# Kernel optimization log

Hardware: AMD Instinct MI355X
Metric: run time of the kernel (lower is better)

The kernel has to match this reference:

```python
import jax, jax.numpy as jnp
import numpy as np

T, NP, NA, NV = 8, 16000, 16000, 200
DIN, H, KA, L = 256, 256, 4, 5
YEARS_TRAIN = (5, 6, 7)
BETA, EPS = 0.5, 1.0
SQRT2 = 1.4142135623730951


def setup_inputs() -> dict:
    key = jax.random.key(0)
    ks = jax.random.split(key, 24)
    s = 0.05
    return {
        'x_paper': jax.random.normal(ks[0], (T, NP, DIN), jnp.float32),
        'x_author': jax.random.normal(ks[1], (T, NA, DIN), jnp.float32),
        'x_venue': jax.random.normal(ks[2], (T, NV, DIN), jnp.float32),
        'neigh_author_idx': jax.random.randint(ks[3], (NP, KA), 0, NA),
        'neigh_venue_idx': jax.random.randint(ks[4], (NP,), 0, NV),
        'y_true': jax.random.uniform(ks[5], (len(YEARS_TRAIN), NP, L), jnp.float32, 0.0, 50.0),
        'W_paper': s * jax.random.normal(ks[6], (DIN, H), jnp.float32),
        'b_paper': jnp.zeros((H,), jnp.float32),
        'W_author': s * jax.random.normal(ks[7], (DIN, H), jnp.float32),
        'b_author': jnp.zeros((H,), jnp.float32),
        'W_venue': s * jax.random.normal(ks[8], (DIN, H), jnp.float32),
        'b_venue': jnp.zeros((H,), jnp.float32),
        'w_meta': jax.random.normal(ks[9], (3,), jnp.float32),
        'Wx': s * jax.random.normal(ks[10], (H, 3 * H), jnp.float32),
        'Wh': s * jax.random.normal(ks[11], (H, 3 * H), jnp.float32),
        'b_gru': jnp.zeros((3 * H,), jnp.float32),
        'W_eta': s * jax.random.normal(ks[12], (H, 1), jnp.float32),
        'b_eta': jnp.zeros((1,), jnp.float32),
        'W_mu': s * jax.random.normal(ks[13], (H, 1), jnp.float32),
        'b_mu': jnp.zeros((1,), jnp.float32),
        'W_sigma': s * jax.random.normal(ks[14], (H, 1), jnp.float32),
        'b_sigma': jnp.zeros((1,), jnp.float32),
    }


def reference(x_paper, x_author, x_venue, neigh_author_idx, neigh_venue_idx, y_true,
              W_paper, b_paper, W_author, b_author, W_venue, b_venue, w_meta,
              Wx, Wh, b_gru, W_eta, b_eta, W_mu, b_mu, W_sigma, b_sigma):
    # --- encoder: per-type linear + ReLU over all T snapshots ---
    emb_p = jax.nn.relu(jnp.einsum('tnd,dh->tnh', x_paper, W_paper) + b_paper)   # [T,NP,H]
    emb_a = jax.nn.relu(jnp.einsum('tnd,dh->tnh', x_author, W_author) + b_author)  # [T,NA,H]
    emb_v = jax.nn.relu(jnp.einsum('tnd,dh->tnh', x_venue, W_venue) + b_venue)   # [T,NV,H]

    # --- temporal smoothing regulariser L_time (all nodes common across years) ---
    l_time = jnp.mean(jnp.stack([
        jnp.mean(jnp.sum((e[1:] - e[:-1]) ** 2, axis=-1)) for e in (emb_p, emb_a, emb_v)
    ]))

    # --- weighted imputer, batched over all papers and all years ---
    w = jax.nn.softmax(w_meta)
    auth_mean = jnp.mean(emb_a[:, neigh_author_idx], axis=2)   # [T,NP,H]
    ven = emb_v[:, neigh_venue_idx]                            # [T,NP,H]
    v_all = w[0] * auth_mean + w[1] * ven + w[2] * emb_p       # [T,NP,H]

    # --- build lookback sequences V_p for all train years at once ---
    yrs = np.array([[t - k for k in range(1, L + 1)] for t in YEARS_TRAIN])  # [3,L]
    V = jnp.transpose(v_all[yrs], (0, 2, 1, 3)).reshape(-1, L, H)  # [B=3*NP, L, H]
    B = V.shape[0]

    # --- ImpactRNN: GRU over the lookback sequence ---
    def gru_step(h, x):
        gx = x @ Wx + b_gru
        gh = h @ Wh
        xr, xz, xn = jnp.split(gx, 3, axis=-1)
        hr, hz, hn = jnp.split(gh, 3, axis=-1)
        r = jax.nn.sigmoid(xr + hr)
        z = jax.nn.sigmoid(xz + hz)
        n = jnp.tanh(xn + r * hn)
        return (1.0 - z) * n + z * h, None

    h0 = jnp.zeros((B, H), V.dtype)
    h_last, _ = jax.lax.scan(gru_step, h0, jnp.swapaxes(V, 0, 1))

    eta = jax.nn.softplus(h_last @ W_eta + b_eta)              # [B,1]
    mu = h_last @ W_mu + b_mu                                  # [B,1]
    sigma = jax.nn.softplus(h_last @ W_sigma + b_sigma) + 1e-3  # [B,1]

    # --- cumulative log-normal citation curve, then per-horizon increments ---
    horizons = jnp.arange(1.0, L + 1.0, dtype=V.dtype)
    zscore = (jnp.log(horizons)[None, :] - mu) / (sigma * SQRT2)
    y_cum = eta * 0.5 * (1.0 + jax.lax.erf(zscore))            # [B,L]
    y_hat = jnp.concatenate([y_cum[:, :1], y_cum[:, 1:] - y_cum[:, :-1]], axis=1)

    l_pred = jnp.mean((jnp.log1p(y_true.reshape(-1, L) + EPS) - jnp.log1p(y_hat)) ** 2)
    return l_pred + BETA * l_time
```

## Files before the change

kernel.cpp:

```cpp
#include <hip/hip_runtime.h>
#include <cmath>

#define NP  16000
#define NV  200
#define HH  256

typedef short short8 __attribute__((ext_vector_type(8)));
typedef float f32x4  __attribute__((ext_vector_type(4)));

__device__ __forceinline__ unsigned short f2b(float f) {
  union { float f; unsigned u; } x; x.f = f;
  unsigned r = x.u + 0x7fffu + ((x.u >> 16) & 1u);
  return (unsigned short)(r >> 16);
}
__device__ __forceinline__ float b2f(unsigned short h) {
  union { unsigned u; float f; } x; x.u = ((unsigned)h) << 16;
  return x.f;
}
__device__ __forceinline__ float b2f_lo(unsigned u) {
  union { unsigned v; float f; } x; x.v = u << 16; return x.f;
}
__device__ __forceinline__ float b2f_hi(unsigned u) {
  union { unsigned v; float f; } x; x.v = u & 0xffff0000u; return x.f;
}
__device__ __forceinline__ unsigned cvt2(float a, float b) {
  unsigned r;
  asm("v_cvt_pk_bf16_f32 %0, %1, %2" : "=v"(r) : "v"(a), "v"(b));
  return r;
}
__device__ __forceinline__ void gld16(const void* g, void* l) {
  __builtin_amdgcn_global_load_lds((const __attribute__((address_space(1))) void*)g,
                                   (__attribute__((address_space(3))) void*)l, 16, 0, 0);
}
__device__ __forceinline__ float sigm(float x) { return 1.f / (1.f + __expf(-x)); }
__device__ __forceinline__ float tanhfast(float x) {
  const float e = __expf(-2.f * fabsf(x));
  const float t = (1.f - e) / (1.f + e);
  return x < 0.f ? -t : t;
}
__device__ __forceinline__ int xcd_swz(int orig, int q, int r) {
  const int xcd = orig & 7, loc = orig >> 3;
  return (xcd < r ? xcd * (q + 1) : r * (q + 1) + (xcd - r) * q) + loc;
}

__global__ __launch_bounds__(256) void packWt(const float* __restrict__ W,
                                              unsigned short* __restrict__ Wt) {
  const int n = blockIdx.x, k = threadIdx.x;
  Wt[n * 256 + k] = f2b(W[k * 256 + n]);
}
__global__ __launch_bounds__(256) void packW2t(const float* __restrict__ Wx,
                                               const float* __restrict__ Wh,
                                               unsigned short* __restrict__ W2t) {
  const int col = blockIdx.x;
  for (int k = threadIdx.x; k < 512; k += 256)
    W2t[(size_t)col * 512 + k] =
        f2b(k < 256 ? Wx[(size_t)k * 768 + col] : Wh[(size_t)(k - 256) * 768 + col]);
}

__global__ __launch_bounds__(512, 2) void embed_all(
    const float* __restrict__ Xp, const float* __restrict__ Xa, const float* __restrict__ Xv,
    const unsigned short* __restrict__ Wtp, const unsigned short* __restrict__ Wta,
    const unsigned short* __restrict__ Wtv,
    const float* __restrict__ bp, const float* __restrict__ ba, const float* __restrict__ bvn,
    unsigned short* __restrict__ Ep, unsigned short* __restrict__ Ea,
    unsigned short* __restrict__ Ev) {
  __shared__ __align__(16) unsigned short lds[24576];
  unsigned short* As = lds;
  unsigned short* Bs = lds + 8192;
  const int t = threadIdx.x, w = t >> 6, l = t & 63;
  const int bid = blockIdx.x;
  const float* Xf; const unsigned short* Wt; const float* bias; unsigned short* E;
  int M, m0;
  if (bid < 1000)      { Xf = Xp; Wt = Wtp; bias = bp;  E = Ep; M = 128000; m0 = bid * 128; }
  else if (bid < 2000) { Xf = Xa; Wt = Wta; bias = ba;  E = Ea; M = 128000; m0 = (bid - 1000) * 128; }
  else                 { Xf = Xv; Wt = Wtv; bias = bvn; E = Ev; M = 1600;   m0 = (bid - 2000) * 128; }
  const int srow = l >> 3, scol = ((l & 7) ^ srow) * 8;
  const int wr = w >> 2, wc = w & 3;
  const int arow = t >> 2, acg = t & 3;
  const int agrow = min(m0 + arow, M - 1);
  const float* aptr = Xf + (size_t)agrow * 256 + acg * 16;

  f32x4 acc[4][4];
#pragma unroll
  for (int i = 0; i < 4; ++i)
#pragma unroll
    for (int j = 0; j < 4; ++j) acc[i][j] = {0.f, 0.f, 0.f, 0.f};

  float4 areg0, areg1, areg2, areg3;
  areg0 = *reinterpret_cast<const float4*>(aptr + 0);
  areg1 = *reinterpret_cast<const float4*>(aptr + 4);
  areg2 = *reinterpret_cast<const float4*>(aptr + 8);
  areg3 = *reinterpret_cast<const float4*>(aptr + 12);

#pragma unroll
  for (int c = 0; c < 4; ++c) {
#pragma unroll
    for (int i = 0; i < 4; ++i) {
      const int seg = 4 * w + i;
      gld16(Wt + (size_t)(8 * seg + srow) * 256 + c * 64 + scol, (void*)(Bs + seg * 512));
    }
    {
      uint4 u0, u1;
      u0.x = cvt2(areg0.x, areg0.y); u0.y = cvt2(areg0.z, areg0.w);
      u0.z = cvt2(areg1.x, areg1.y); u0.w = cvt2(areg1.z, areg1.w);
      u1.x = cvt2(areg2.x, areg2.y); u1.y = cvt2(areg2.z, areg2.w);
      u1.z = cvt2(areg3.x, areg3.y); u1.w = cvt2(areg3.z, areg3.w);
      const int s0 = (acg * 2) ^ (arow & 7), s1 = (acg * 2 + 1) ^ (arow & 7);
      *reinterpret_cast<uint4*>(As + arow * 64 + s0 * 8) = u0;
      *reinterpret_cast<uint4*>(As + arow * 64 + s1 * 8) = u1;
    }
    if (c < 3) {
      const float* np = aptr + (c + 1) * 64;
      areg0 = *reinterpret_cast<const float4*>(np + 0);
      areg1 = *reinterpret_cast<const float4*>(np + 4);
      areg2 = *reinterpret_cast<const float4*>(np + 8);
      areg3 = *reinterpret_cast<const float4*>(np + 12);
    }
    __syncthreads();
#pragma unroll
    for (int ks = 0; ks < 2; ++ks) {
      short8 av[4], bv[4];
#pragma unroll
      for (int mi = 0; mi < 4; ++mi) {
        const int r = wr * 64 + mi * 16 + (l & 15);
        const int slot = (ks * 4 + (l >> 4)) ^ (r & 7);
        av[mi] = *reinterpret_cast<const short8*>(As + r * 64 + slot * 8);
      }
#pragma unroll
      for (int nj = 0; nj < 4; ++nj) {
        const int r = wc * 64 + nj * 16 + (l & 15);
        const int slot = (ks * 4 + (l >> 4)) ^ (r & 7);
        bv[nj] = *reinterpret_cast<const short8*>(Bs + r * 64 + slot * 8);
      }
#pragma unroll
      for (int mi = 0; mi < 4; ++mi)
#pragma unroll
        for (int nj = 0; nj < 4; ++nj)
          acc[mi][nj] = __builtin_amdgcn_mfma_f32_16x16x32_bf16(av[mi], bv[nj], acc[mi][nj], 0, 0, 0);
    }
    __syncthreads();
  }

  unsigned short* ep = lds + w * 2560;
  const int grow = m0 + wr * 64 + l;
#pragma unroll
  for (int p = 0; p < 2; ++p) {
#pragma unroll
    for (int nj2 = 0; nj2 < 2; ++nj2) {
      const int nj = 2 * p + nj2;
      const int colg = wc * 64 + nj * 16 + (l & 15);
      const float bvv = bias[colg];
#pragma unroll
      for (int mi = 0; mi < 4; ++mi)
#pragma unroll
        for (int e = 0; e < 4; ++e) {
          const int rl = mi * 16 + (l >> 4) * 4 + e;
          ep[rl * 40 + nj2 * 16 + (l & 15)] = f2b(fmaxf(acc[mi][nj][e] + bvv, 0.f));
        }
    }
    __syncthreads();
    if (grow < M) {
#pragma unroll
      for (int j = 0; j < 4; ++j) {
        const uint4 v = *reinterpret_cast<const uint4*>(ep + l * 40 + j * 8);
        *reinterpret_cast<uint4*>(E + (size_t)grow * 256 + wc * 64 + p * 32 + j * 8) = v;
      }
    }
    __syncthreads();
  }
}

__global__ __launch_bounds__(256, 2) void gx_gemm(const unsigned short* __restrict__ Abf,
                                                  const unsigned short* __restrict__ W2t,
                                                  const float* __restrict__ bias,
                                                  unsigned short* __restrict__ GX) {
  __shared__ __align__(16) unsigned short lds[16384];
  unsigned short* As = lds;
  unsigned short* Bs = lds + 8192;
  const int t = threadIdx.x, w = t >> 6, l = t & 63;
  const int work = xcd_swz(blockIdx.x, 656, 2);
  const int m0 = (work / 6) * 128, n0 = (work % 6) * 128;
  const int srow = l >> 3;
  const int scol = ((l & 7) ^ srow) * 8;
  f32x4 acc[4][4];
#pragma unroll
  for (int i = 0; i < 4; ++i)
#pragma unroll
    for (int j = 0; j < 4; ++j) acc[i][j] = {0.f, 0.f, 0.f, 0.f};
  const int mrow0 = 64 * (w >> 1), ncol0 = 64 * (w & 1);

#pragma unroll
  for (int c = 0; c < 4; ++c) {
#pragma unroll
    for (int i = 0; i < 4; ++i) {
      const int seg = 4 * w + i;
      gld16(Abf + (size_t)(m0 + 8 * seg + srow) * 256 + c * 64 + scol, (void*)(As + seg * 512));
    }
#pragma unroll
    for (int i = 0; i < 4; ++i) {
      const int seg = 4 * w + i;
      gld16(W2t + (size_t)(n0 + 8 * seg + srow) * 512 + c * 64 + scol, (void*)(Bs + seg * 512));
    }
    __syncthreads();
#pragma unroll
    for (int ks = 0; ks < 2; ++ks) {
      short8 av[4], bv[4];
#pragma unroll
      for (int mi = 0; mi < 4; ++mi) {
        const int r = mrow0 + mi * 16 + (l & 15);
        const int slot = (ks * 4 + (l >> 4)) ^ (r & 7);
        av[mi] = *reinterpret_cast<const short8*>(As + r * 64 + slot * 8);
      }
#pragma unroll
      for (int nj = 0; nj < 4; ++nj) {
        const int r = ncol0 + nj * 16 + (l & 15);
        const int slot = (ks * 4 + (l >> 4)) ^ (r & 7);
        bv[nj] = *reinterpret_cast<const short8*>(Bs + r * 64 + slot * 8);
      }
#pragma unroll
      for (int mi = 0; mi < 4; ++mi)
#pragma unroll
        for (int nj = 0; nj < 4; ++nj)
          acc[mi][nj] = __builtin_amdgcn_mfma_f32_16x16x32_bf16(av[mi], bv[nj], acc[mi][nj], 0, 0, 0);
    }
    __syncthreads();
  }
  unsigned short* ep = lds + w * 2560;
  const int grow = m0 + mrow0 + l;
#pragma unroll
  for (int p = 0; p < 2; ++p) {
#pragma unroll
    for (int nj2 = 0; nj2 < 2; ++nj2) {
      const int nj = 2 * p + nj2;
      const int colg = n0 + ncol0 + nj * 16 + (l & 15);
      const float bvv = bias[colg];
#pragma unroll
      for (int mi = 0; mi < 4; ++mi)
#pragma unroll
        for (int e = 0; e < 4; ++e) {
          const int rl = mi * 16 + (l >> 4) * 4 + e;
          ep[rl * 40 + nj2 * 16 + (l & 15)] = f2b(acc[mi][nj][e] + bvv);
        }
    }
    __syncthreads();
#pragma unroll
    for (int j = 0; j < 4; ++j) {
      const uint4 v = *reinterpret_cast<const uint4*>(ep + l * 40 + j * 8);
      *reinterpret_cast<uint4*>(GX + (size_t)grow * 768 + n0 + ncol0 + p * 32 + j * 8) = v;
    }
    __syncthreads();
  }
}

__global__ __launch_bounds__(256) void ltime_kernel(const unsigned short* __restrict__ ep,
                                                    const unsigned short* __restrict__ ea,
                                                    const unsigned short* __restrict__ ev,
                                                    float* __restrict__ partials) {
  const unsigned PO = 3584000u, VO = 44800u;
  const unsigned TOT = 2u * PO + VO;
  const unsigned SL = 512000u, SLV = 6400u;
  const float wbig = 1.f / (3.f * 7.f * 16000.f);
  const float wsmall = 1.f / (3.f * 7.f * 200.f);
  float local = 0.f;
  for (unsigned i = blockIdx.x * 256u + threadIdx.x; i < TOT; i += gridDim.x * 256u) {
    const unsigned short* base; unsigned off, sl; float wgt;
    if (i < 2u * PO) { base = (i < PO) ? ep : ea; off = (i < PO) ? i : i - PO; sl = SL; wgt = wbig; }
    else             { base = ev; off = i - 2u * PO; sl = SLV; wgt = wsmall; }
    const uint4 u0 = *reinterpret_cast<const uint4*>(base + (size_t)off * 8);
    const uint4 u1 = *reinterpret_cast<const uint4*>(base + (size_t)(off + sl) * 8);
    float s = 0.f, d;
    d = b2f_lo(u1.x) - b2f_lo(u0.x); s += d * d;
    d = b2f_hi(u1.x) - b2f_hi(u0.x); s += d * d;
    d = b2f_lo(u1.y) - b2f_lo(u0.y); s += d * d;
    d = b2f_hi(u1.y) - b2f_hi(u0.y); s += d * d;
    d = b2f_lo(u1.z) - b2f_lo(u0.z); s += d * d;
    d = b2f_hi(u1.z) - b2f_hi(u0.z); s += d * d;
    d = b2f_lo(u1.w) - b2f_lo(u0.w); s += d * d;
    d = b2f_hi(u1.w) - b2f_hi(u0.w); s += d * d;
    local += wgt * s;
  }
  __shared__ float red[256];
  red[threadIdx.x] = local;
  __syncthreads();
  for (int s = 128; s > 0; s >>= 1) {
    if (threadIdx.x < s) red[threadIdx.x] += red[threadIdx.x + s];
    __syncthreads();
  }
  if (threadIdx.x == 0) partials[blockIdx.x] = red[0];
}

__global__ __launch_bounds__(256) void vall_kernel(const unsigned short* __restrict__ ep,
                                                   const unsigned short* __restrict__ ea,
                                                   const unsigned short* __restrict__ ev,
                                                   const int* __restrict__ aidx,
                                                   const int* __restrict__ vidx,
                                                   const float* __restrict__ wm,
                                                   unsigned short* __restrict__ vall) {
  const int w = threadIdx.x >> 6, l = threadIdx.x & 63;
  const int n = blockIdx.x * 4 + w;
  float w0 = wm[0], w1 = wm[1], w2 = wm[2];
  const float mx = fmaxf(w0, fmaxf(w1, w2));
  const float e0 = expf(w0 - mx), e1 = expf(w1 - mx), e2 = expf(w2 - mx);
  const float inv = 1.f / (e0 + e1 + e2);
  w0 = e0 * inv; w1 = e1 * inv; w2 = e2 * inv;
  const int a0 = aidx[n * 4 + 0], a1 = aidx[n * 4 + 1];
  const int a2 = aidx[n * 4 + 2], a3 = aidx[n * 4 + 3];
  const int vn = vidx[n];
  const int cb = l * 4;
  for (int t = 0; t < 7; ++t) {
    const size_t tb = (size_t)t * NP * HH;
    const uint2 ua0 = *reinterpret_cast<const uint2*>(ea + tb + (size_t)a0 * HH + cb);
    const uint2 ua1 = *reinterpret_cast<const uint2*>(ea + tb + (size_t)a1 * HH + cb);
    const uint2 ua2 = *reinterpret_cast<const uint2*>(ea + tb + (size_t)a2 * HH + cb);
    const uint2 ua3 = *reinterpret_cast<const uint2*>(ea + tb + (size_t)a3 * HH + cb);
    const uint2 uv  = *reinterpret_cast<const uint2*>(ev + (size_t)t * NV * HH + (size_t)vn * HH + cb);
    const uint2 up  = *reinterpret_cast<const uint2*>(ep + tb + (size_t)n * HH + cb);
    float o[4];
    o[0] = w0 * 0.25f * (b2f_lo(ua0.x) + b2f_lo(ua1.x) + b2f_lo(ua2.x) + b2f_lo(ua3.x)) + w1 * b2f_lo(uv.x) + w2 * b2f_lo(up.x);
    o[1] = w0 * 0.25f * (b2f_hi(ua0.x) + b2f_hi(ua1.x) + b2f_hi(ua2.x) + b2f_hi(ua3.x)) + w1 * b2f_hi(uv.x) + w2 * b2f_hi(up.x);
    o[2] = w0 * 0.25f * (b2f_lo(ua0.y) + b2f_lo(ua1.y) + b2f_lo(ua2.y) + b2f_lo(ua3.y)) + w1 * b2f_lo(uv.y) + w2 * b2f_lo(up.y);
    o[3] = w0 * 0.25f * (b2f_hi(ua0.y) + b2f_hi(ua1.y) + b2f_hi(ua2.y) + b2f_hi(ua3.y)) + w1 * b2f_hi(uv.y) + w2 * b2f_hi(up.y);
    uint2 ov; ov.x = cvt2(o[0], o[1]); ov.y = cvt2(o[2], o[3]);
    *reinterpret_cast<uint2*>(vall + tb + (size_t)n * HH + cb) = ov;
  }
}

__global__ __launch_bounds__(256) void gru_h0(const unsigned short* __restrict__ GX,
                                              unsigned short* __restrict__ H0) {
  const int idx = blockIdx.x * 256 + threadIdx.x;
  const int hrow = idx >> 6, jq = idx & 63;
  const int g = (hrow >= 32000) ? 2 : (hrow >= 16000 ? 1 : 0);
  const int n = hrow - g * 16000;
  const size_t gxrow = (size_t)(4 + g) * 16000 + n;
  const unsigned short* gp = GX + gxrow * 768 + jq * 4;
  const uint2 uz = *reinterpret_cast<const uint2*>(gp + 256);
  const uint2 un = *reinterpret_cast<const uint2*>(gp + 512);
  float h[4];
  h[0] = (1.f - sigm(b2f_lo(uz.x))) * tanhfast(b2f_lo(un.x));
  h[1] = (1.f - sigm(b2f_hi(uz.x))) * tanhfast(b2f_hi(un.x));
  h[2] = (1.f - sigm(b2f_lo(uz.y))) * tanhfast(b2f_lo(un.y));
  h[3] = (1.f - sigm(b2f_hi(uz.y))) * tanhfast(b2f_hi(un.y));
  uint2 o; o.x = cvt2(h[0], h[1]); o.y = cvt2(h[2], h[3]);
  *reinterpret_cast<uint2*>(H0 + (size_t)hrow * 256 + jq * 4) = o;
}

__global__ __launch_bounds__(512, 2) void gru_hstep(const unsigned short* __restrict__ GX,
                                                    const unsigned short* __restrict__ W2t,
                                                    const unsigned short* __restrict__ Hsrc,
                                                    unsigned short* __restrict__ Hdst,
                                                    int lstep) {
  __shared__ __align__(16) unsigned short lds[32768];
  unsigned short* As = lds;
  unsigned short* Bs = lds + 8192;
  const int t = threadIdx.x, w = t >> 6, l = t & 63;
  const int work = xcd_swz(blockIdx.x, 93, 6);
  const int bx = work >> 1, jb = work & 1;
  const int m0 = bx * 128, j0 = jb * 128;
  const int g = bx / 125;
  const size_t gxRowBase = (size_t)(4 + g - lstep) * 16000 + (size_t)(m0 - g * 16000);
  const int srow = l >> 3;
  const int scol = ((l & 7) ^ srow) * 8;
  const int wr = w >> 2, wj = w & 3;
  f32x4 acc[3][4][2];
#pragma unroll
  for (int gate = 0; gate < 3; ++gate)
#pragma unroll
    for (int mi = 0; mi < 4; ++mi)
#pragma unroll
      for (int nj = 0; nj < 2; ++nj) acc[gate][mi][nj] = {0.f, 0.f, 0.f, 0.f};

#pragma unroll
  for (int c = 0; c < 4; ++c) {
#pragma unroll
    for (int i = 0; i < 2; ++i) {
      const int seg = w * 2 + i;
      gld16(Hsrc + (size_t)(m0 + 8 * seg + srow) * 256 + c * 64 + scol, (void*)(As + seg * 512));
    }
#pragma unroll
    for (int i = 0; i < 6; ++i) {
      const int seg = w * 6 + i;
      const int tilerow = 8 * seg + srow;
      const int gate = tilerow >> 7, jj = tilerow & 127;
      gld16(W2t + (size_t)(gate * 256 + j0 + jj) * 512 + 256 + c * 64 + scol,
            (void*)(Bs + seg * 512));
    }
    __syncthreads();
#pragma unroll
    for (int ks = 0; ks < 2; ++ks) {
      short8 av[4];
#pragma unroll
      for (int mi = 0; mi < 4; ++mi) {
        const int r = wr * 64 + mi * 16 + (l & 15);
        const int slot = (ks * 4 + (l >> 4)) ^ (r & 7);
        av[mi] = *reinterpret_cast<const short8*>(As + r * 64 + slot * 8);
      }
#pragma unroll
      for (int gate = 0; gate < 3; ++gate) {
        short8 bv0, bv1;
        {
          const int r0 = gate * 128 + wj * 32 + (l & 15);
          const int s0 = (ks * 4 + (l >> 4)) ^ (r0 & 7);
          bv0 = *reinterpret_cast<const short8*>(Bs + r0 * 64 + s0 * 8);
          const int r1 = r0 + 16;
          const int s1 = (ks * 4 + (l >> 4)) ^ (r1 & 7);
          bv1 = *reinterpret_cast<const short8*>(Bs + r1 * 64 + s1 * 8);
        }
#pragma unroll
        for (int mi = 0; mi < 4; ++mi) {
          acc[gate][mi][0] = __builtin_amdgcn_mfma_f32_16x16x32_bf16(av[mi], bv0, acc[gate][mi][0], 0, 0, 0);
          acc[gate][mi][1] = __builtin_amdgcn_mfma_f32_16x16x32_bf16(av[mi], bv1, acc[gate][mi][1], 0, 0, 0);
        }
      }
    }
    __syncthreads();
  }
  unsigned short* ep = lds + w * 2560;
#pragma unroll
  for (int nj = 0; nj < 2; ++nj) {
    const int jcol = j0 + wj * 32 + nj * 16 + (l & 15);
#pragma unroll
    for (int mi = 0; mi < 4; ++mi) {
#pragma unroll
      for (int e = 0; e < 4; ++e) {
        const int rib = wr * 64 + mi * 16 + (l >> 4) * 4 + e;
        const size_t hidx = (size_t)(m0 + rib) * 256 + jcol;
        const size_t gxoff = (gxRowBase + rib) * 768 + jcol;
        const float aR = acc[0][mi][nj][e] + b2f(GX[gxoff]);
        const float aZ = acc[1][mi][nj][e] + b2f(GX[gxoff + 256]);
        const float hn = acc[2][mi][nj][e];
        const float xn = b2f(GX[gxoff + 512]);
        const float rg = sigm(aR);
        const float zg = sigm(aZ);
        const float ng = tanhfast(xn + rg * hn);
        const float ho = b2f(Hsrc[hidx]);
        const int rl = mi * 16 + (l >> 4) * 4 + e;
        ep[rl * 40 + nj * 16 + (l & 15)] = f2b((1.f - zg) * ng + zg * ho);
      }
    }
  }
  __syncthreads();
  {
    const int grow = m0 + wr * 64 + l;
#pragma unroll
    for (int j = 0; j < 4; ++j) {
      const uint4 v = *reinterpret_cast<const uint4*>(ep + l * 40 + j * 8);
      *reinterpret_cast<uint4*>(Hdst + (size_t)grow * 256 + j0 + wj * 32 + j * 8) = v;
    }
  }
}

__device__ inline float softplusf(float x) { return x > 20.f ? x : log1pf(expf(x)); }

__global__ __launch_bounds__(256) void head_kernel(const unsigned short* __restrict__ Hbuf,
                                                   const float* __restrict__ We, const float* __restrict__ be,
                                                   const float* __restrict__ Wm, const float* __restrict__ bmu,
                                                   const float* __restrict__ Ws, const float* __restrict__ bsg,
                                                   const float* __restrict__ yt,
                                                   float* __restrict__ partials) {
  __shared__ float sWe[256], sWm[256], sWs[256];
  const int t = threadIdx.x;
  sWe[t] = We[t]; sWm[t] = Wm[t]; sWs[t] = Ws[t];
  __syncthreads();
  const int row = blockIdx.x * 256 + t;
  float loss = 0.f;
  if (row < 48000) {
    const unsigned short* h = Hbuf + (size_t)row * HH;
    float pe = 0.f, pm = 0.f, ps = 0.f;
#pragma unroll 4
    for (int k0 = 0; k0 < 256; k0 += 8) {
      const uint4 u = *reinterpret_cast<const uint4*>(h + k0);
      const float hv[8] = {b2f_lo(u.x), b2f_hi(u.x), b2f_lo(u.y), b2f_hi(u.y),
                           b2f_lo(u.z), b2f_hi(u.z), b2f_lo(u.w), b2f_hi(u.w)};
#pragma unroll
      for (int q = 0; q < 8; ++q) {
        const int k = k0 + q;
        pe += hv[q] * sWe[k]; pm += hv[q] * sWm[k]; ps += hv[q] * sWs[k];
      }
    }
    const float eta = softplusf(pe + be[0]);
    const float mu  = pm + bmu[0];
    const float sg  = softplusf(ps + bsg[0]) + 0.001f;
    const float inv = 1.f / (sg * 1.41421356237309515f);
    float prev = 0.f;
#pragma unroll
    for (int hz = 1; hz <= 5; ++hz) {
      const float z  = (logf((float)hz) - mu) * inv;
      const float yc = eta * 0.5f * (1.f + erff(z));
      const float yh = yc - prev; prev = yc;
      const float d  = log1pf(yt[(size_t)row * 5 + (hz - 1)] + 1.0f) - log1pf(yh);
      loss += d * d;
    }
  }
  __shared__ float red[256];
  red[t] = loss;
  __syncthreads();
  for (int s = 128; s > 0; s >>= 1) {
    if (t < s) red[t] += red[t + s];
    __syncthreads();
  }
  if (t == 0) partials[blockIdx.x] = red[0];
}

__global__ __launch_bounds__(256) void final_kernel(const float* __restrict__ lt,
                                                    const float* __restrict__ lp,
                                                    float* __restrict__ out) {
  __shared__ float r1[256], r2[256];
  float s1 = 0.f, s2 = 0.f;
  for (int i = threadIdx.x; i < 1024; i += 256) s1 += lt[i];
  for (int i = threadIdx.x; i < 188; i += 256) s2 += lp[i];
  r1[threadIdx.x] = s1; r2[threadIdx.x] = s2;
  __syncthreads();
  for (int s = 128; s > 0; s >>= 1) {
    if (threadIdx.x < s) { r1[threadIdx.x] += r1[threadIdx.x + s]; r2[threadIdx.x] += r2[threadIdx.x + s]; }
    __syncthreads();
  }
  if (threadIdx.x == 0) out[0] = r2[0] / 240000.f + 0.5f * r1[0];
}

extern "C" void kernel_launch(void* const* d_in, const int* in_sizes, int n_in,
                              void* d_out, int out_size, void* d_ws, size_t ws_size,
                              hipStream_t stream) {
  (void)in_sizes; (void)n_in; (void)out_size; (void)ws_size;
  const float* x_paper  = (const float*)d_in[0];
  const float* x_author = (const float*)d_in[1];
  const float* x_venue  = (const float*)d_in[2];
  const int*   aidx     = (const int*)d_in[3];
  const int*   vidx     = (const int*)d_in[4];
  const float* y_true   = (const float*)d_in[5];
  const float* W_paper  = (const float*)d_in[6];
  const float* b_paper  = (const float*)d_in[7];
  const float* W_author = (const float*)d_in[8];
  const float* b_author = (const float*)d_in[9];
  const float* W_venue  = (const float*)d_in[10];
  const float* b_venue  = (const float*)d_in[11];
  const float* w_meta   = (const float*)d_in[12];
  const float* Wx       = (const float*)d_in[13];
  const float* Wh       = (const float*)d_in[14];
  const float* b_gru    = (const float*)d_in[15];
  const float* W_eta    = (const float*)d_in[16];
  const float* b_eta    = (const float*)d_in[17];
  const float* W_mu     = (const float*)d_in[18];
  const float* b_mu     = (const float*)d_in[19];
  const float* W_sigma  = (const float*)d_in[20];
  const float* b_sigma  = (const float*)d_in[21];

  unsigned short* p = (unsigned short*)d_ws;
  unsigned short* va16 = p;  p += (size_t)7 * NP * 256;
  unsigned short* Hb0  = p;  p += (size_t)48000 * 256;
  unsigned short* Hb1  = p;  p += (size_t)48000 * 256;
  unsigned short* W2t  = p;  p += (size_t)768 * 512;
  unsigned short* GX   = p;  p += (size_t)112000 * 768;
  float* ltp = (float*)p;
  float* lpp = ltp + 1024;
  unsigned short* ep16 = GX;
  unsigned short* ea16 = ep16 + (size_t)8 * NP * 256;
  unsigned short* ev16 = ea16 + (size_t)8 * NP * 256;
  unsigned short* Wtp  = ev16 + (size_t)8 * NV * 256;
  unsigned short* Wta  = Wtp + 65536;
  unsigned short* Wtv  = Wta + 65536;

  packWt<<<256, 256, 0, stream>>>(W_paper,  Wtp);
  packWt<<<256, 256, 0, stream>>>(W_author, Wta);
  packWt<<<256, 256, 0, stream>>>(W_venue,  Wtv);
  packW2t<<<768, 256, 0, stream>>>(Wx, Wh, W2t);

  embed_all<<<2013, 512, 0, stream>>>(x_paper, x_author, x_venue, Wtp, Wta, Wtv,
                                      b_paper, b_author, b_venue, ep16, ea16, ev16);

  ltime_kernel<<<1024, 256, 0, stream>>>(ep16, ea16, ev16, ltp);
  vall_kernel<<<NP / 4, 256, 0, stream>>>(ep16, ea16, ev16, aidx, vidx, w_meta, va16);

  gx_gemm<<<5250, 256, 0, stream>>>(va16, W2t, b_gru, GX);

  gru_h0<<<12000, 256, 0, stream>>>(GX, Hb0);
  gru_hstep<<<750, 512, 0, stream>>>(GX, W2t, Hb0, Hb1, 1);
  gru_hstep<<<750, 512, 0, stream>>>(GX, W2t, Hb1, Hb0, 2);
  gru_hstep<<<750, 512, 0, stream>>>(GX, W2t, Hb0, Hb1, 3);
  gru_hstep<<<750, 512, 0, stream>>>(GX, W2t, Hb1, Hb0, 4);

  head_kernel<<<188, 256, 0, stream>>>(Hb0, W_eta, b_eta, W_mu, b_mu, W_sigma, b_sigma,
                                       y_true, lpp);
  final_kernel<<<1, 256, 0, stream>>>(ltp, lpp, (float*)d_out);
}
```

Baseline: 581.9 us.

## Retile embed and GX GEMMs to 64-row tiles with single-pass epilogue

The embedding GEMM moves from 128x256 tiles to 64x256 tiles, doubling the block count and halving per-wave accumulators and LDS. The GX GEMM moves from 128x128 tiles with 256 threads to 64x256 tiles with 512 threads. Both epilogues now stage the whole tile in padded LDS once and write full rows, replacing the two-pass per-wave staging. The aim is more occupancy and less sync in the epilogue, at the cost of reloading the full B weight tile more often relative to A. The M-bound clamp is dropped; the venue blocks divide exactly into 64-row tiles.

```diff
diff --git a/kernel.cpp b/kernel.cpp
--- a/kernel.cpp
+++ b/kernel.cpp
@@ -57,40 +57,36 @@
         f2b(k < 256 ? Wx[(size_t)k * 768 + col] : Wh[(size_t)(k - 256) * 768 + col]);
 }
 
-__global__ __launch_bounds__(512, 2) void embed_all(
+__global__ __launch_bounds__(512) void embed_all(
     const float* __restrict__ Xp, const float* __restrict__ Xa, const float* __restrict__ Xv,
     const unsigned short* __restrict__ Wtp, const unsigned short* __restrict__ Wta,
     const unsigned short* __restrict__ Wtv,
     const float* __restrict__ bp, const float* __restrict__ ba, const float* __restrict__ bvn,
     unsigned short* __restrict__ Ep, unsigned short* __restrict__ Ea,
     unsigned short* __restrict__ Ev) {
-  __shared__ __align__(16) unsigned short lds[24576];
+  __shared__ __align__(16) unsigned short lds[20480];
   unsigned short* As = lds;
-  unsigned short* Bs = lds + 8192;
+  unsigned short* Bs = lds + 4096;
   const int t = threadIdx.x, w = t >> 6, l = t & 63;
   const int bid = blockIdx.x;
   const float* Xf; const unsigned short* Wt; const float* bias; unsigned short* E;
-  int M, m0;
-  if (bid < 1000)      { Xf = Xp; Wt = Wtp; bias = bp;  E = Ep; M = 128000; m0 = bid * 128; }
-  else if (bid < 2000) { Xf = Xa; Wt = Wta; bias = ba;  E = Ea; M = 128000; m0 = (bid - 1000) * 128; }
-  else                 { Xf = Xv; Wt = Wtv; bias = bvn; E = Ev; M = 1600;   m0 = (bid - 2000) * 128; }
+  int m0;
+  if (bid < 2000)      { Xf = Xp; Wt = Wtp; bias = bp;  E = Ep; m0 = bid * 64; }
+  else if (bid < 4000) { Xf = Xa; Wt = Wta; bias = ba;  E = Ea; m0 = (bid - 2000) * 64; }
+  else                 { Xf = Xv; Wt = Wtv; bias = bvn; E = Ev; m0 = (bid - 4000) * 64; }
   const int srow = l >> 3, scol = ((l & 7) ^ srow) * 8;
-  const int wr = w >> 2, wc = w & 3;
-  const int arow = t >> 2, acg = t & 3;
-  const int agrow = min(m0 + arow, M - 1);
-  const float* aptr = Xf + (size_t)agrow * 256 + acg * 16;
-
-  f32x4 acc[4][4];
-#pragma unroll
-  for (int i = 0; i < 4; ++i)
+  const int wrow = (w >> 2) * 32, wcol = (w & 3) * 64;
+  const int arow = t >> 3, aseg = t & 7;
+  const float* aptr = Xf + (size_t)(m0 + arow) * 256 + aseg * 8;
+
+  f32x4 acc[2][4];
+#pragma unroll
+  for (int i = 0; i < 2; ++i)
 #pragma unroll
     for (int j = 0; j < 4; ++j) acc[i][j] = {0.f, 0.f, 0.f, 0.f};
 
-  float4 areg0, areg1, areg2, areg3;
-  areg0 = *reinterpret_cast<const float4*>(aptr + 0);
-  areg1 = *reinterpret_cast<const float4*>(aptr + 4);
-  areg2 = *reinterpret_cast<const float4*>(aptr + 8);
-  areg3 = *reinterpret_cast<const float4*>(aptr + 12);
+  float4 a0 = *reinterpret_cast<const float4*>(aptr);
+  float4 a1 = *reinterpret_cast<const float4*>(aptr + 4);
 
 #pragma unroll
   for (int c = 0; c < 4; ++c) {
@@ -100,40 +96,35 @@
       gld16(Wt + (size_t)(8 * seg + srow) * 256 + c * 64 + scol, (void*)(Bs + seg * 512));
     }
     {
-      uint4 u0, u1;
-      u0.x = cvt2(areg0.x, areg0.y); u0.y = cvt2(areg0.z, areg0.w);
-      u0.z = cvt2(areg1.x, areg1.y); u0.w = cvt2(areg1.z, areg1.w);
-      u1.x = cvt2(areg2.x, areg2.y); u1.y = cvt2(areg2.z, areg2.w);
-      u1.z = cvt2(areg3.x, areg3.y); u1.w = cvt2(areg3.z, areg3.w);
-      const int s0 = (acg * 2) ^ (arow & 7), s1 = (acg * 2 + 1) ^ (arow & 7);
-      *reinterpret_cast<uint4*>(As + arow * 64 + s0 * 8) = u0;
-      *reinterpret_cast<uint4*>(As + arow * 64 + s1 * 8) = u1;
+      uint4 u;
+      u.x = cvt2(a0.x, a0.y); u.y = cvt2(a0.z, a0.w);
+      u.z = cvt2(a1.x, a1.y); u.w = cvt2(a1.z, a1.w);
+      const int slot = aseg ^ (arow & 7);
+      *reinterpret_cast<uint4*>(As + arow * 64 + slot * 8) = u;
     }
     if (c < 3) {
       const float* np = aptr + (c + 1) * 64;
-      areg0 = *reinterpret_cast<const float4*>(np + 0);
-      areg1 = *reinterpret_cast<const float4*>(np + 4);
-      areg2 = *reinterpret_cast<const float4*>(np + 8);
-      areg3 = *reinterpret_cast<const float4*>(np + 12);
+      a0 = *reinterpret_cast<const float4*>(np);
+      a1 = *reinterpret_cast<const float4*>(np + 4);
     }
     __syncthreads();
 #pragma unroll
     for (int ks = 0; ks < 2; ++ks) {
-      short8 av[4], bv[4];
-#pragma unroll
-      for (int mi = 0; mi < 4; ++mi) {
-        const int r = wr * 64 + mi * 16 + (l & 15);
+      short8 av[2], bv[4];
+#pragma unroll
+      for (int mi = 0; mi < 2; ++mi) {
+        const int r = wrow + mi * 16 + (l & 15);
         const int slot = (ks * 4 + (l >> 4)) ^ (r & 7);
         av[mi] = *reinterpret_cast<const short8*>(As + r * 64 + slot * 8);
       }
 #pragma unroll
       for (int nj = 0; nj < 4; ++nj) {
-        const int r = wc * 64 + nj * 16 + (l & 15);
+        const int r = wcol + nj * 16 + (l & 15);
         const int slot = (ks * 4 + (l >> 4)) ^ (r & 7);
         bv[nj] = *reinterpret_cast<const short8*>(Bs + r * 64 + slot * 8);
       }
 #pragma unroll
-      for (int mi = 0; mi < 4; ++mi)
+      for (int mi = 0; mi < 2; ++mi)
 #pragma unroll
         for (int nj = 0; nj < 4; ++nj)
           acc[mi][nj] = __builtin_amdgcn_mfma_f32_16x16x32_bf16(av[mi], bv[nj], acc[mi][nj], 0, 0, 0);
@@ -141,61 +132,53 @@
     __syncthreads();
   }
 
-  unsigned short* ep = lds + w * 2560;
-  const int grow = m0 + wr * 64 + l;
-#pragma unroll
-  for (int p = 0; p < 2; ++p) {
-#pragma unroll
-    for (int nj2 = 0; nj2 < 2; ++nj2) {
-      const int nj = 2 * p + nj2;
-      const int colg = wc * 64 + nj * 16 + (l & 15);
-      const float bvv = bias[colg];
-#pragma unroll
-      for (int mi = 0; mi < 4; ++mi)
-#pragma unroll
-        for (int e = 0; e < 4; ++e) {
-          const int rl = mi * 16 + (l >> 4) * 4 + e;
-          ep[rl * 40 + nj2 * 16 + (l & 15)] = f2b(fmaxf(acc[mi][nj][e] + bvv, 0.f));
-        }
-    }
-    __syncthreads();
-    if (grow < M) {
-#pragma unroll
-      for (int j = 0; j < 4; ++j) {
-        const uint4 v = *reinterpret_cast<const uint4*>(ep + l * 40 + j * 8);
-        *reinterpret_cast<uint4*>(E + (size_t)grow * 256 + wc * 64 + p * 32 + j * 8) = v;
-      }
-    }
-    __syncthreads();
-  }
-}
-
-__global__ __launch_bounds__(256, 2) void gx_gemm(const unsigned short* __restrict__ Abf,
-                                                  const unsigned short* __restrict__ W2t,
-                                                  const float* __restrict__ bias,
-                                                  unsigned short* __restrict__ GX) {
-  __shared__ __align__(16) unsigned short lds[16384];
+#pragma unroll
+  for (int nj = 0; nj < 4; ++nj) {
+    const int col = wcol + nj * 16 + (l & 15);
+    const float bvv = bias[col];
+#pragma unroll
+    for (int mi = 0; mi < 2; ++mi)
+#pragma unroll
+      for (int e = 0; e < 4; ++e) {
+        const int row = wrow + mi * 16 + (l >> 4) * 4 + e;
+        lds[row * 264 + col] = f2b(fmaxf(acc[mi][nj][e] + bvv, 0.f));
+      }
+  }
+  __syncthreads();
+  {
+    const int r2 = t >> 3, s2 = t & 7;
+    const unsigned short* src = lds + r2 * 264 + s2 * 32;
+    const uint4 v0 = *reinterpret_cast<const uint4*>(src);
+    const uint4 v1 = *reinterpret_cast<const uint4*>(src + 8);
+    const uint4 v2 = *reinterpret_cast<const uint4*>(src + 16);
+    const uint4 v3 = *reinterpret_cast<const uint4*>(src + 24);
+    uint4* dst = reinterpret_cast<uint4*>(E + (size_t)(m0 + r2) * 256 + s2 * 32);
+    dst[0] = v0; dst[1] = v1; dst[2] = v2; dst[3] = v3;
+  }
+}
+
+__global__ __launch_bounds__(512) void gx_gemm(const unsigned short* __restrict__ Abf,
+                                               const unsigned short* __restrict__ W2t,
+                                               const float* __restrict__ bias,
+                                               unsigned short* __restrict__ GX) {
+  __shared__ __align__(16) unsigned short lds[20480];
   unsigned short* As = lds;
-  unsigned short* Bs = lds + 8192;
+  unsigned short* Bs = lds + 4096;
   const int t = threadIdx.x, w = t >> 6, l = t & 63;
   const int work = xcd_swz(blockIdx.x, 656, 2);
-  const int m0 = (work / 6) * 128, n0 = (work % 6) * 128;
-  const int srow = l >> 3;
-  const int scol = ((l & 7) ^ srow) * 8;
-  f32x4 acc[4][4];
-#pragma unroll
-  for (int i = 0; i < 4; ++i)
+  const int m0 = (work / 3) * 64, n0 = (work % 3) * 256;
+  const int srow = l >> 3, scol = ((l & 7) ^ srow) * 8;
+  const int wrow = (w >> 2) * 32, wcol = (w & 3) * 64;
+
+  f32x4 acc[2][4];
+#pragma unroll
+  for (int i = 0; i < 2; ++i)
 #pragma unroll
     for (int j = 0; j < 4; ++j) acc[i][j] = {0.f, 0.f, 0.f, 0.f};
-  const int mrow0 = 64 * (w >> 1), ncol0 = 64 * (w & 1);
 
 #pragma unroll
   for (int c = 0; c < 4; ++c) {
-#pragma unroll
-    for (int i = 0; i < 4; ++i) {
-      const int seg = 4 * w + i;
-      gld16(Abf + (size_t)(m0 + 8 * seg + srow) * 256 + c * 64 + scol, (void*)(As + seg * 512));
-    }
+    gld16(Abf + (size_t)(m0 + 8 * w + srow) * 256 + c * 64 + scol, (void*)(As + w * 512));
 #pragma unroll
     for (int i = 0; i < 4; ++i) {
       const int seg = 4 * w + i;
@@ -204,51 +187,50 @@
     __syncthreads();
 #pragma unroll
     for (int ks = 0; ks < 2; ++ks) {
-      short8 av[4], bv[4];
-#pragma unroll
-      for (int mi = 0; mi < 4; ++mi) {
-        const int r = mrow0 + mi * 16 + (l & 15);
+      short8 av[2], bv[4];
+#pragma unroll
+      for (int mi = 0; mi < 2; ++mi) {
+        const int r = wrow + mi * 16 + (l & 15);
         const int slot = (ks * 4 + (l >> 4)) ^ (r & 7);
         av[mi] = *reinterpret_cast<const short8*>(As + r * 64 + slot * 8);
       }
 #pragma unroll
       for (int nj = 0; nj < 4; ++nj) {
-        const int r = ncol0 + nj * 16 + (l & 15);
+        const int r = wcol + nj * 16 + (l & 15);
         const int slot = (ks * 4 + (l >> 4)) ^ (r & 7);
         bv[nj] = *reinterpret_cast<const short8*>(Bs + r * 64 + slot * 8);
       }
 #pragma unroll
-      for (int mi = 0; mi < 4; ++mi)
+      for (int mi = 0; mi < 2; ++mi)
 #pragma unroll
         for (int nj = 0; nj < 4; ++nj)
           acc[mi][nj] = __builtin_amdgcn_mfma_f32_16x16x32_bf16(av[mi], bv[nj], acc[mi][nj], 0, 0, 0);
     }
     __syncthreads();
   }
-  unsigned short* ep = lds + w * 2560;
-  const int grow = m0 + mrow0 + l;
-#pragma unroll
-  for (int p = 0; p < 2; ++p) {
-#pragma unroll
-    for (int nj2 = 0; nj2 < 2; ++nj2) {
-      const int nj = 2 * p + nj2;
-      const int colg = n0 + ncol0 + nj * 16 + (l & 15);
-      const float bvv = bias[colg];
-#pragma unroll
-      for (int mi = 0; mi < 4; ++mi)
-#pragma unroll
-        for (int e = 0; e < 4; ++e) {
-          const int rl = mi * 16 + (l >> 4) * 4 + e;
-          ep[rl * 40 + nj2 * 16 + (l & 15)] = f2b(acc[mi][nj][e] + bvv);
-        }
-    }
-    __syncthreads();
-#pragma unroll
-    for (int j = 0; j < 4; ++j) {
-      const uint4 v = *reinterpret_cast<const uint4*>(ep + l * 40 + j * 8);
-      *reinterpret_cast<uint4*>(GX + (size_t)grow * 768 + n0 + ncol0 + p * 32 + j * 8) = v;
-    }
-    __syncthreads();
+
+#pragma unroll
+  for (int nj = 0; nj < 4; ++nj) {
+    const int col = wcol + nj * 16 + (l & 15);
+    const float bvv = bias[n0 + col];
+#pragma unroll
+    for (int mi = 0; mi < 2; ++mi)
+#pragma unroll
+      for (int e = 0; e < 4; ++e) {
+        const int row = wrow + mi * 16 + (l >> 4) * 4 + e;
+        lds[row * 264 + col] = f2b(acc[mi][nj][e] + bvv);
+      }
+  }
+  __syncthreads();
+  {
+    const int r2 = t >> 3, s2 = t & 7;
+    const unsigned short* src = lds + r2 * 264 + s2 * 32;
+    const uint4 v0 = *reinterpret_cast<const uint4*>(src);
+    const uint4 v1 = *reinterpret_cast<const uint4*>(src + 8);
+    const uint4 v2 = *reinterpret_cast<const uint4*>(src + 16);
+    const uint4 v3 = *reinterpret_cast<const uint4*>(src + 24);
+    uint4* dst = reinterpret_cast<uint4*>(GX + (size_t)(m0 + r2) * 768 + n0 + s2 * 32);
+    dst[0] = v0; dst[1] = v1; dst[2] = v2; dst[3] = v3;
   }
 }
 
@@ -564,13 +546,13 @@
   packWt<<<256, 256, 0, stream>>>(W_venue,  Wtv);
   packW2t<<<768, 256, 0, stream>>>(Wx, Wh, W2t);
 
-  embed_all<<<2013, 512, 0, stream>>>(x_paper, x_author, x_venue, Wtp, Wta, Wtv,
+  embed_all<<<4025, 512, 0, stream>>>(x_paper, x_author, x_venue, Wtp, Wta, Wtv,
                                       b_paper, b_author, b_venue, ep16, ea16, ev16);
 
   ltime_kernel<<<1024, 256, 0, stream>>>(ep16, ea16, ev16, ltp);
   vall_kernel<<<NP / 4, 256, 0, stream>>>(ep16, ea16, ev16, aidx, vidx, w_meta, va16);
 
-  gx_gemm<<<5250, 256, 0, stream>>>(va16, W2t, b_gru, GX);
+  gx_gemm<<<5250, 512, 0, stream>>>(va16, W2t, b_gru, GX);
 
   gru_h0<<<12000, 256, 0, stream>>>(GX, Hb0);
   gru_hstep<<<750, 512, 0, stream>>>(GX, W2t, Hb0, Hb1, 1);
```

Measured after the change: 558.7 us. 4.0% less time.
